# Performance work log

Measured on AMD Instinct MI355X. Metric: run time of the kernel, lower is better.

The kernel has to match this reference:

```python
import jax, jax.numpy as jnp
import numpy as np

B = 64          # num_graphs per batch
ADJ = 1000      # adj_shape (nodes per graph)
N = B * ADJ     # total nodes
E = 1 << 20     # edges
M = 32000       # selected (batch, node) pairs
D_IN = 128
D_OUT = 128


def setup_inputs() -> dict:
    key = jax.random.key(0)
    ks = jax.random.split(key, 12)
    inp = {
        "x0": jax.random.normal(ks[0], (N, D_IN), jnp.float32),
        "x1": jax.random.normal(ks[1], (N, D_IN), jnp.float32),
        "edge_index": jax.random.randint(ks[2], (2, E), 0, N, jnp.int64),
        "b_idx0": jax.random.randint(ks[3], (M,), 0, B, jnp.int64),
        "n_idx0": jax.random.randint(ks[4], (M,), 0, ADJ, jnp.int64),
        "b_idx1": jax.random.randint(ks[5], (M,), 0, B, jnp.int64),
        "n_idx1": jax.random.randint(ks[6], (M,), 0, ADJ, jnp.int64),
        "W1": jax.random.normal(ks[7], (D_IN, D_IN), jnp.float32) / np.sqrt(D_IN),
        "b1": jnp.zeros((D_IN,), jnp.float32),
        "W2": jax.random.normal(ks[8], (D_IN, D_IN), jnp.float32) / np.sqrt(D_IN),
        "b2": jnp.zeros((D_IN,), jnp.float32),
        "Wl": jax.random.normal(ks[9], (D_IN, D_OUT), jnp.float32) / np.sqrt(D_IN),
        "bl": jnp.zeros((D_OUT,), jnp.float32),
        "Wfi": jax.random.normal(ks[10], (D_IN, D_OUT), jnp.float32) / np.sqrt(D_IN),
        "bfi": jnp.zeros((D_OUT,), jnp.float32),
    }
    return inp


def _gnn_layer(h, edge_index, W, b):
    # GCN-style message passing: gather source features, scatter-sum to dst,
    # then linear project.  h: [N, d]
    msgs = h[edge_index[0]]                                    # [E, d] gather
    agg = jax.ops.segment_sum(msgs, edge_index[1], num_segments=N)  # [N, d]
    return agg @ W + b


def reference(x0, x1, edge_index, b_idx0, n_idx0, b_idx1, n_idx1,
              W1, b1, W2, b2, Wl, bl, Wfi, bfi):
    # branch i == 0: raw features -> 2D gather -> fc_in
    d0 = x0.reshape(B, ADJ, -1)[b_idx0, n_idx0]                # [M, D_IN]
    d0 = d0 @ Wfi + bfi                                        # [M, D_OUT]

    # branch i == 1 (observ=True): gnn1 -> gnn2 -> 2D gather -> linear
    # (dropout omitted for deterministic reference; p=0.2 at train time)
    h = _gnn_layer(x1, edge_index, W1, b1)
    h = _gnn_layer(h, edge_index, W2, b2)
    d1 = h.reshape(B, ADJ, -1)[b_idx1, n_idx1]                 # [M, D_IN]
    d1 = d1 @ Wl + bl                                          # [M, D_OUT]

    return jnp.stack([d0, d1])                                 # [2, M, D_OUT]
```

## Files before the change

kernel.cpp:

```cpp
#include <hip/hip_runtime.h>
#include <hip/hip_bf16.h>


#define B_    64
#define ADJ_  1000
#define N_    64000
#define E_    (1 << 20)
#define M_    32000
#define DV    128
#define CAP   64
#define RANGES 8
#define RSPAN  (N_ / RANGES)
#define CHUNKS 512
#define EPB    (E_ / CHUNKS)

typedef __attribute__((ext_vector_type(8))) short short8v;
typedef __attribute__((ext_vector_type(4))) float float4v;

__device__ __forceinline__ float u2f(unsigned int u) {
  union { unsigned int i; float f; } x; x.i = u; return x.f;
}
__device__ __forceinline__ unsigned short f2bf(float f) {
  union { float f; unsigned int i; } x; x.f = f;
  unsigned int r = x.i + 0x7fffu + ((x.i >> 16) & 1u);
  return (unsigned short)(r >> 16);
}
__device__ __forceinline__ unsigned int pack_bf2(float a, float b) {
  __hip_bfloat162 h = __float22bfloat162_rn(float2{a, b});
  union { __hip_bfloat162 h; unsigned int u; } c; c.h = h;
  return c.u;
}

__global__ __launch_bounds__(256)
void fill_buckets(const int* __restrict__ ei, int* __restrict__ counts,
                  unsigned short* __restrict__ bucket) {
  int r  = blockIdx.x & (RANGES - 1);
  int c  = blockIdx.x >> 3;
  int lo = r * RSPAN, hi = lo + RSPAN;
  int base = c * EPB;
#pragma unroll
  for (int i = 0; i < EPB / 256; i++) {
    int e = base + i * 256 + threadIdx.x;
    int dst = ei[E_ + e];
    if (dst >= lo && dst < hi) {
      int src = ei[e];
      int pos = atomicAdd(&counts[dst], 1);
      if (pos < CAP) bucket[dst * CAP + pos] = (unsigned short)src;
    }
  }
}

__global__ __launch_bounds__(256)
void aggregate_bf16(const unsigned int* __restrict__ x,
                    const int* __restrict__ counts,
                    const unsigned short* __restrict__ bucket,
                    const float* __restrict__ bias,
                    float* __restrict__ out) {
  int w    = (blockIdx.x * 256 + threadIdx.x) >> 6;
  int lane = threadIdx.x & 63;
  if (w >= N_) return;
  int cnt = counts[w]; cnt = min(cnt, CAP);
  int mysrc = (int)bucket[w * CAP + lane];
  float2 acc; acc.x = bias[lane * 2]; acc.y = bias[lane * 2 + 1];

  int d = 0;
  for (; d + 4 <= cnt; d += 4) {
    int s0 = __shfl(mysrc, d, 64);
    int s1 = __shfl(mysrc, d + 1, 64);
    int s2 = __shfl(mysrc, d + 2, 64);
    int s3 = __shfl(mysrc, d + 3, 64);
    unsigned int u0 = x[(size_t)s0 * 64 + lane];
    unsigned int u1 = x[(size_t)s1 * 64 + lane];
    unsigned int u2 = x[(size_t)s2 * 64 + lane];
    unsigned int u3 = x[(size_t)s3 * 64 + lane];
    acc.x += (u2f(u0 << 16) + u2f(u1 << 16)) + (u2f(u2 << 16) + u2f(u3 << 16));
    acc.y += (u2f(u0 & 0xffff0000u) + u2f(u1 & 0xffff0000u))
           + (u2f(u2 & 0xffff0000u) + u2f(u3 & 0xffff0000u));
  }
  for (; d < cnt; d++) {
    int s = __shfl(mysrc, d, 64);
    unsigned int u = x[(size_t)s * 64 + lane];
    acc.x += u2f(u << 16);
    acc.y += u2f(u & 0xffff0000u);
  }
  ((float2*)out)[(size_t)w * 64 + lane] = acc;
}

template<bool GATHER, bool OUTBF16, bool HASBIAS>
__global__ __launch_bounds__(256)
void gemm_mfma(const float* __restrict__ in, const float* __restrict__ W,
               const float* __restrict__ bias, void* __restrict__ out_,
               const int* __restrict__ bidx, const int* __restrict__ nidx) {
  __shared__ unsigned short Bs[8 * 4 * 64 * 8];
  int tid = threadIdx.x;

#pragma unroll 8
  for (int i = 0; i < 64; i++) {
    int g = i * 256 + tid;
    int k = g >> 7, n = g & 127;
    int addr = ((((n >> 4) * 4 + (k >> 5)) * 64 + ((k >> 3) & 3) * 16 + (n & 15)) << 3)
             + (k & 7);
    Bs[addr] = f2bf(W[g]);
  }
  __syncthreads();

  int lane = tid & 63;
  int wv   = tid >> 6;
  int m    = lane & 15;
  int q    = lane >> 4;
  int rbase = blockIdx.x * 64 + wv * 16;
  int r     = rbase + m;

  size_t ir;
  if (GATHER) ir = (size_t)bidx[r] * ADJ_ + nidx[r];
  else        ir = (size_t)r;
  const float* arow = in + ir * DV;

  short8v af[4];
#pragma unroll
  for (int kc = 0; kc < 4; kc++) {
    const float4* p = (const float4*)(arow + kc * 32 + q * 8);
    float4 f0 = p[0], f1 = p[1];
    union { short8v s; unsigned int u[4]; } t;
    t.u[0] = pack_bf2(f0.x, f0.y);
    t.u[1] = pack_bf2(f0.z, f0.w);
    t.u[2] = pack_bf2(f1.x, f1.y);
    t.u[3] = pack_bf2(f1.z, f1.w);
    af[kc] = t.s;
  }

  float4v acc[8];
#pragma unroll
  for (int nb = 0; nb < 8; nb++) acc[nb] = (float4v){0.f, 0.f, 0.f, 0.f};

#pragma unroll
  for (int nb = 0; nb < 8; nb++) {
#pragma unroll
    for (int kc = 0; kc < 4; kc++) {
      short8v bf = *(const short8v*)(Bs + (((nb * 4 + kc) * 64 + lane) << 3));
      acc[nb] = __builtin_amdgcn_mfma_f32_16x16x32_bf16(af[kc], bf, acc[nb], 0, 0, 0);
    }
  }

#pragma unroll
  for (int nb = 0; nb < 8; nb++) {
    float bvn = HASBIAS ? bias[nb * 16 + m] : 0.f;
    int col = nb * 16 + m;
#pragma unroll
    for (int i = 0; i < 4; i++) {
      int row = rbase + q * 4 + i;
      float v = acc[nb][i] + bvn;
      if (OUTBF16) ((unsigned short*)out_)[(size_t)row * DV + col] = f2bf(v);
      else         ((float*)out_)[(size_t)row * DV + col] = v;
    }
  }
}

extern "C" void kernel_launch(void* const* d_in, const int* in_sizes, int n_in,
                              void* d_out, int out_size, void* d_ws, size_t ws_size,
                              hipStream_t stream) {
  const float* x0  = (const float*)d_in[0];
  const float* x1  = (const float*)d_in[1];
  const int*   ei  = (const int*)  d_in[2];
  const int*   b0  = (const int*)  d_in[3];
  const int*   n0i = (const int*)  d_in[4];
  const int*   b1  = (const int*)  d_in[5];
  const int*   n1i = (const int*)  d_in[6];
  const float* W1  = (const float*)d_in[7];
  const float* bb1 = (const float*)d_in[8];
  const float* W2  = (const float*)d_in[9];
  const float* bb2 = (const float*)d_in[10];
  const float* Wl  = (const float*)d_in[11];
  const float* bl  = (const float*)d_in[12];
  const float* Wfi = (const float*)d_in[13];
  const float* bfi = (const float*)d_in[14];
  float* out = (float*)d_out;

  unsigned int*   t_bf   = (unsigned int*)d_ws;
  float*          h      = (float*)(t_bf + (size_t)N_ * 64);
  int*            counts = (int*)(h + (size_t)N_ * DV);
  unsigned short* bucket = (unsigned short*)(counts + N_);

  hipMemsetAsync(counts, 0, N_ * sizeof(int), stream);
  fill_buckets<<<CHUNKS * RANGES, 256, 0, stream>>>(ei, counts, bucket);

  gemm_mfma<false, true, false><<<N_ / 64, 256, 0, stream>>>(x1, W1, nullptr, t_bf, nullptr, nullptr);
  aggregate_bf16<<<N_ / 4, 256, 0, stream>>>(t_bf, counts, bucket, bb1, h);

  gemm_mfma<false, true, false><<<N_ / 64, 256, 0, stream>>>(h, W2, nullptr, t_bf, nullptr, nullptr);
  aggregate_bf16<<<N_ / 4, 256, 0, stream>>>(t_bf, counts, bucket, bb2, h);

  gemm_mfma<true, false, true><<<M_ / 64, 256, 0, stream>>>(x0, Wfi, bfi, out, b0, n0i);

  gemm_mfma<true, false, true><<<M_ / 64, 256, 0, stream>>>(h, Wl, bl, out + (size_t)M_ * DV, b1, n1i);
}
```

Measured before the change: 293.2 us.

## Fuse bucketing with first GEMMs, aggregate only selected nodes in layer two

Merges edge bucketing, the layer-1 projection and the x0 gather-GEMM into one heterogeneous launch so independent work can overlap. Vectorises the edge loads in bucket filling. Stores intermediate activations in bf16 instead of fp32, halving their traffic. The second aggregation now runs only for the M selected rows, with the final linear fed from that compact buffer, which skips aggregating unused nodes. The costs are extra bf16 rounding of intermediates and the risk that mixed block roles in the fused kernel load-balance poorly.

New measurement: 269.5 us. 8.1% less time.

```diff
diff --git a/kernel.cpp b/kernel.cpp
--- a/kernel.cpp
+++ b/kernel.cpp
@@ -31,37 +31,145 @@
   return c.u;
 }
 
+__device__ __forceinline__ void fill_part(const int* __restrict__ ei,
+                                          int* __restrict__ counts,
+                                          unsigned short* __restrict__ bucket,
+                                          int c, int r) {
+  const int* srcA = ei;
+  const int* dstA = ei + E_;
+  int lo = r * RSPAN;
+  int t4 = c * EPB + (int)threadIdx.x * 4;
+  int4 d0 = *(const int4*)(dstA + t4);
+  int4 s0 = *(const int4*)(srcA + t4);
+  int4 d1 = *(const int4*)(dstA + t4 + 1024);
+  int4 s1 = *(const int4*)(srcA + t4 + 1024);
+#define PROC(D, S) do {                                                \
+    if ((unsigned)((D) - lo) < (unsigned)RSPAN) {                      \
+      int pos = atomicAdd(&counts[(D)], 1);                            \
+      if (pos < CAP) bucket[(D) * CAP + pos] = (unsigned short)(S);    \
+    } } while (0)
+  PROC(d0.x, s0.x); PROC(d0.y, s0.y); PROC(d0.z, s0.z); PROC(d0.w, s0.w);
+  PROC(d1.x, s1.x); PROC(d1.y, s1.y); PROC(d1.z, s1.z); PROC(d1.w, s1.w);
+#undef PROC
+}
+
+template<bool GATHER, bool ABF16, bool OUTBF16, bool HASBIAS>
+__device__ __forceinline__ void gemm_tile(const void* __restrict__ in,
+                                          const float* __restrict__ W,
+                                          const float* __restrict__ bias,
+                                          void* __restrict__ out_, int tile,
+                                          const int* __restrict__ bidx,
+                                          const int* __restrict__ nidx,
+                                          unsigned short* __restrict__ Bs) {
+  int tid = threadIdx.x;
+#pragma unroll 8
+  for (int i = 0; i < 64; i++) {
+    int g = i * 256 + tid;
+    int k = g >> 7, n = g & 127;
+    int addr = ((((n >> 4) * 4 + (k >> 5)) * 64 + ((k >> 3) & 3) * 16 + (n & 15)) << 3)
+             + (k & 7);
+    Bs[addr] = f2bf(W[g]);
+  }
+  __syncthreads();
+
+  int lane = tid & 63;
+  int wv   = tid >> 6;
+  int m    = lane & 15;
+  int q    = lane >> 4;
+  int rbase = tile * 64 + wv * 16;
+  int r     = rbase + m;
+
+  size_t ir;
+  if (GATHER) ir = (size_t)bidx[r] * ADJ_ + nidx[r];
+  else        ir = (size_t)r;
+
+  short8v af[4];
+  if (ABF16) {
+    const unsigned short* arow = (const unsigned short*)in + ir * DV;
+#pragma unroll
+    for (int kc = 0; kc < 4; kc++)
+      af[kc] = *(const short8v*)(arow + kc * 32 + q * 8);
+  } else {
+    const float* arow = (const float*)in + ir * DV;
+#pragma unroll
+    for (int kc = 0; kc < 4; kc++) {
+      const float4* p = (const float4*)(arow + kc * 32 + q * 8);
+      float4 f0 = p[0], f1 = p[1];
+      union { short8v s; unsigned int u[4]; } t;
+      t.u[0] = pack_bf2(f0.x, f0.y);
+      t.u[1] = pack_bf2(f0.z, f0.w);
+      t.u[2] = pack_bf2(f1.x, f1.y);
+      t.u[3] = pack_bf2(f1.z, f1.w);
+      af[kc] = t.s;
+    }
+  }
+
+  float4v acc[8];
+#pragma unroll
+  for (int nb = 0; nb < 8; nb++) acc[nb] = (float4v){0.f, 0.f, 0.f, 0.f};
+#pragma unroll
+  for (int nb = 0; nb < 8; nb++)
+#pragma unroll
+    for (int kc = 0; kc < 4; kc++) {
+      short8v bf = *(const short8v*)(Bs + (((nb * 4 + kc) * 64 + lane) << 3));
+      acc[nb] = __builtin_amdgcn_mfma_f32_16x16x32_bf16(af[kc], bf, acc[nb], 0, 0, 0);
+    }
+
+#pragma unroll
+  for (int nb = 0; nb < 8; nb++) {
+    float bvn = HASBIAS ? bias[nb * 16 + m] : 0.f;
+    int col = nb * 16 + m;
+#pragma unroll
+    for (int i = 0; i < 4; i++) {
+      int row = rbase + q * 4 + i;
+      float v = acc[nb][i] + bvn;
+      if (OUTBF16) ((unsigned short*)out_)[(size_t)row * DV + col] = f2bf(v);
+      else         ((float*)out_)[(size_t)row * DV + col] = v;
+    }
+  }
+}
+
 __global__ __launch_bounds__(256)
-void fill_buckets(const int* __restrict__ ei, int* __restrict__ counts,
-                  unsigned short* __restrict__ bucket) {
-  int r  = blockIdx.x & (RANGES - 1);
-  int c  = blockIdx.x >> 3;
-  int lo = r * RSPAN, hi = lo + RSPAN;
-  int base = c * EPB;
-#pragma unroll
-  for (int i = 0; i < EPB / 256; i++) {
-    int e = base + i * 256 + threadIdx.x;
-    int dst = ei[E_ + e];
-    if (dst >= lo && dst < hi) {
-      int src = ei[e];
-      int pos = atomicAdd(&counts[dst], 1);
-      if (pos < CAP) bucket[dst * CAP + pos] = (unsigned short)src;
-    }
-  }
-}
-
+void k1_fused(const int* __restrict__ ei, int* __restrict__ counts,
+              unsigned short* __restrict__ bucket,
+              const float* __restrict__ x1, const float* __restrict__ W1,
+              unsigned int* __restrict__ t_bf,
+              const float* __restrict__ x0, const float* __restrict__ Wfi,
+              const float* __restrict__ bfi, float* __restrict__ out0,
+              const int* __restrict__ b0, const int* __restrict__ n0i) {
+  __shared__ unsigned short Bs[16384];
+  int g = blockIdx.x >> 4, rem = blockIdx.x & 15;
+  if (rem < 8) { fill_part(ei, counts, bucket, g, rem); return; }
+  int o = g * 8 + rem - 8;
+  if (o < 1000)
+    gemm_tile<false, false, true, false>(x1, W1, nullptr, t_bf, o, nullptr, nullptr, Bs);
+  else if (o < 1500)
+    gemm_tile<true, false, false, true>(x0, Wfi, bfi, out0, o - 1000, b0, n0i, Bs);
+}
+
+template<bool GATHER, bool ABF16, bool OUTBF16, bool HASBIAS>
 __global__ __launch_bounds__(256)
-void aggregate_bf16(const unsigned int* __restrict__ x,
-                    const int* __restrict__ counts,
-                    const unsigned short* __restrict__ bucket,
-                    const float* __restrict__ bias,
-                    float* __restrict__ out) {
+void gemm_k(const void* __restrict__ in, const float* __restrict__ W,
+            const float* __restrict__ bias, void* __restrict__ out_,
+            const int* __restrict__ bidx, const int* __restrict__ nidx) {
+  __shared__ unsigned short Bs[16384];
+  gemm_tile<GATHER, ABF16, OUTBF16, HASBIAS>(in, W, bias, out_, blockIdx.x, bidx, nidx, Bs);
+}
+
+template<bool OUTBF16, bool SEL>
+__global__ __launch_bounds__(256)
+void aggregate_k(const unsigned int* __restrict__ x,
+                 const int* __restrict__ counts,
+                 const unsigned short* __restrict__ bucket,
+                 const float* __restrict__ bias, void* __restrict__ out_,
+                 const int* __restrict__ bidx, const int* __restrict__ nidx) {
   int w    = (blockIdx.x * 256 + threadIdx.x) >> 6;
   int lane = threadIdx.x & 63;
-  if (w >= N_) return;
-  int cnt = counts[w]; cnt = min(cnt, CAP);
-  int mysrc = (int)bucket[w * CAP + lane];
-  float2 acc; acc.x = bias[lane * 2]; acc.y = bias[lane * 2 + 1];
+  int node = SEL ? (bidx[w] * ADJ_ + nidx[w]) : w;
+  int cnt = counts[node]; cnt = min(cnt, CAP);
+  int mysrc = (int)bucket[node * CAP + lane];
+  float2 bv = ((const float2*)bias)[lane];
+  float2 acc; acc.x = bv.x; acc.y = bv.y;
 
   int d = 0;
   for (; d + 4 <= cnt; d += 4) {
@@ -83,77 +191,8 @@
     acc.x += u2f(u << 16);
     acc.y += u2f(u & 0xffff0000u);
   }
-  ((float2*)out)[(size_t)w * 64 + lane] = acc;
-}
-
-template<bool GATHER, bool OUTBF16, bool HASBIAS>
-__global__ __launch_bounds__(256)
-void gemm_mfma(const float* __restrict__ in, const float* __restrict__ W,
-               const float* __restrict__ bias, void* __restrict__ out_,
-               const int* __restrict__ bidx, const int* __restrict__ nidx) {
-  __shared__ unsigned short Bs[8 * 4 * 64 * 8];
-  int tid = threadIdx.x;
-
-#pragma unroll 8
-  for (int i = 0; i < 64; i++) {
-    int g = i * 256 + tid;
-    int k = g >> 7, n = g & 127;
-    int addr = ((((n >> 4) * 4 + (k >> 5)) * 64 + ((k >> 3) & 3) * 16 + (n & 15)) << 3)
-             + (k & 7);
-    Bs[addr] = f2bf(W[g]);
-  }
-  __syncthreads();
-
-  int lane = tid & 63;
-  int wv   = tid >> 6;
-  int m    = lane & 15;
-  int q    = lane >> 4;
-  int rbase = blockIdx.x * 64 + wv * 16;
-  int r     = rbase + m;
-
-  size_t ir;
-  if (GATHER) ir = (size_t)bidx[r] * ADJ_ + nidx[r];
-  else        ir = (size_t)r;
-  const float* arow = in + ir * DV;
-
-  short8v af[4];
-#pragma unroll
-  for (int kc = 0; kc < 4; kc++) {
-    const float4* p = (const float4*)(arow + kc * 32 + q * 8);
-    float4 f0 = p[0], f1 = p[1];
-    union { short8v s; unsigned int u[4]; } t;
-    t.u[0] = pack_bf2(f0.x, f0.y);
-    t.u[1] = pack_bf2(f0.z, f0.w);
-    t.u[2] = pack_bf2(f1.x, f1.y);
-    t.u[3] = pack_bf2(f1.z, f1.w);
-    af[kc] = t.s;
-  }
-
-  float4v acc[8];
-#pragma unroll
-  for (int nb = 0; nb < 8; nb++) acc[nb] = (float4v){0.f, 0.f, 0.f, 0.f};
-
-#pragma unroll
-  for (int nb = 0; nb < 8; nb++) {
-#pragma unroll
-    for (int kc = 0; kc < 4; kc++) {
-      short8v bf = *(const short8v*)(Bs + (((nb * 4 + kc) * 64 + lane) << 3));
-      acc[nb] = __builtin_amdgcn_mfma_f32_16x16x32_bf16(af[kc], bf, acc[nb], 0, 0, 0);
-    }
-  }
-
-#pragma unroll
-  for (int nb = 0; nb < 8; nb++) {
-    float bvn = HASBIAS ? bias[nb * 16 + m] : 0.f;
-    int col = nb * 16 + m;
-#pragma unroll
-    for (int i = 0; i < 4; i++) {
-      int row = rbase + q * 4 + i;
-      float v = acc[nb][i] + bvn;
-      if (OUTBF16) ((unsigned short*)out_)[(size_t)row * DV + col] = f2bf(v);
-      else         ((float*)out_)[(size_t)row * DV + col] = v;
-    }
-  }
+  if (OUTBF16) ((unsigned int*)out_)[(size_t)w * 64 + lane] = pack_bf2(acc.x, acc.y);
+  else         ((float2*)out_)[(size_t)w * 64 + lane] = acc;
 }
 
 extern "C" void kernel_launch(void* const* d_in, const int* in_sizes, int n_in,
@@ -177,20 +216,23 @@
   float* out = (float*)d_out;
 
   unsigned int*   t_bf   = (unsigned int*)d_ws;
-  float*          h      = (float*)(t_bf + (size_t)N_ * 64);
-  int*            counts = (int*)(h + (size_t)N_ * DV);
+  unsigned int*   h_bf   = t_bf + (size_t)N_ * 64;
+  unsigned int*   sel_bf = h_bf + (size_t)N_ * 64;
+  int*            counts = (int*)(sel_bf + (size_t)M_ * 64);
   unsigned short* bucket = (unsigned short*)(counts + N_);
 
   hipMemsetAsync(counts, 0, N_ * sizeof(int), stream);
-  fill_buckets<<<CHUNKS * RANGES, 256, 0, stream>>>(ei, counts, bucket);
-
-  gemm_mfma<false, true, false><<<N_ / 64, 256, 0, stream>>>(x1, W1, nullptr, t_bf, nullptr, nullptr);
-  aggregate_bf16<<<N_ / 4, 256, 0, stream>>>(t_bf, counts, bucket, bb1, h);
-
-  gemm_mfma<false, true, false><<<N_ / 64, 256, 0, stream>>>(h, W2, nullptr, t_bf, nullptr, nullptr);
-  aggregate_bf16<<<N_ / 4, 256, 0, stream>>>(t_bf, counts, bucket, bb2, h);
-
-  gemm_mfma<true, false, true><<<M_ / 64, 256, 0, stream>>>(x0, Wfi, bfi, out, b0, n0i);
-
-  gemm_mfma<true, false, true><<<M_ / 64, 256, 0, stream>>>(h, Wl, bl, out + (size_t)M_ * DV, b1, n1i);
-}
+
+  k1_fused<<<512 * 16, 256, 0, stream>>>(ei, counts, bucket, x1, W1, t_bf,
+                                         x0, Wfi, bfi, out, b0, n0i);
+
+  aggregate_k<true, false><<<N_ / 4, 256, 0, stream>>>(t_bf, counts, bucket, bb1,
+                                                       h_bf, nullptr, nullptr);
+  gemm_k<false, true, true, false><<<N_ / 64, 256, 0, stream>>>(h_bf, W2, nullptr,
+                                                                t_bf, nullptr, nullptr);
+  aggregate_k<true, true><<<M_ / 4, 256, 0, stream>>>(t_bf, counts, bucket, bb2,
+                                                      sel_bf, b1, n1i);
+  gemm_k<false, true, false, true><<<M_ / 64, 256, 0, stream>>>(sel_bf, Wl, bl,
+                                                                out + (size_t)M_ * DV,
+                                                                nullptr, nullptr);
+}
```
